# Kernel tuning notes

Measured on AMD Instinct MI355X. Metric: run time of the kernel, lower is better.

## Reference

```python
import jax, jax.numpy as jnp
import numpy as np

B, S, D = 4, 2048, 512   # batch, seq_len, hidden_size
H, HD = 1, 512           # num_heads (must be 1 given the view), head_size
ALPHA, BW, A = 2.0, 512.0, 0.5
EPS = 1e-12              # F.normalize / cdist-grad stabilizer


def setup_inputs() -> dict:
    key = jax.random.key(0)
    ks = jax.random.split(key, 7)
    s = 1.0 / np.sqrt(D)  # keep q,k,v at unit scale like trained weights
    return {
        "x": jax.random.normal(ks[0], (B, S, D), jnp.float32),
        "Wq": jax.random.normal(ks[1], (HD, D), jnp.float32) * s,
        "bq": jax.random.normal(ks[2], (HD,), jnp.float32) * 0.01,
        "Wk": jax.random.normal(ks[3], (HD, D), jnp.float32) * s,
        "bk": jax.random.normal(ks[4], (HD,), jnp.float32) * 0.01,
        "Wv": jax.random.normal(ks[5], (HD, D), jnp.float32) * s,
        "bv": jax.random.normal(ks[6], (HD,), jnp.float32) * 0.01,
    }


def reference(x, Wq, bq, Wk, bk, Wv, bv):
    # projections, then (B, H, S, HD)
    q = (x @ Wq.T + bq).reshape(B, S, H, HD).transpose(0, 2, 1, 3)
    k = (x @ Wk.T + bk).reshape(B, S, H, HD).transpose(0, 2, 1, 3)
    v = (x @ Wv.T + bv).reshape(B, S, H, HD).transpose(0, 2, 1, 3)

    # torch.cdist(q, k, p=2): pairwise Euclidean distance, shape (B, H, S, S)
    sq = ((q * q).sum(-1)[..., :, None]
          + (k * k).sum(-1)[..., None, :]
          - 2.0 * jnp.einsum('bhsd,bhtd->bhst', q, k))
    g_dist = jnp.sqrt(jnp.maximum(sq, EPS))

    # alpha >= 2 branch: exp(-(g / sqrt(bw))**(alpha/(alpha-1)))
    attn_score = jnp.exp(-(g_dist / jnp.sqrt(BW)) ** (ALPHA / (ALPHA - 1.0)))

    # bistochastic (Sinkhorn-like) renormalization, a > 0 branch
    N_R = attn_score.sum(-1)   # row sums  (B, H, S)
    N_C = attn_score.sum(-2)   # col sums  (B, H, S)
    K_tilde = (N_R ** (-A))[..., :, None] * attn_score * (N_C ** (-A))[..., None, :]

    # F.normalize(K_tilde, p=1, dim=3); entries are nonnegative so |.| == .
    probs = K_tilde / jnp.maximum(K_tilde.sum(-1, keepdims=True), EPS)

    # dropout prob = 0.0 -> identity
    out = jnp.einsum('bhst,bhtd->bhsd', probs, v)
    return out, probs
```

## Files before the change

### kernel.cpp

```cpp
#include <hip/hip_runtime.h>
#include <hip/hip_bf16.h>

typedef short short8 __attribute__((ext_vector_type(8)));
typedef short short4v __attribute__((ext_vector_type(4)));
typedef float f32x4 __attribute__((ext_vector_type(4)));

#define S_LEN 2048
#define DIM   512
#define NBATCH 4

typedef unsigned short ushort_t;

__device__ __forceinline__ float b2f(unsigned short u) {
    union { unsigned u; float f; } x; x.u = ((unsigned)u) << 16; return x.f;
}
__device__ __forceinline__ unsigned short f2b(float f) {
    union { float f; unsigned u; } x; x.f = f;
    unsigned r = x.u + 0x7FFFu + ((x.u >> 16) & 1u);
    return (unsigned short)(r >> 16);
}
__device__ __forceinline__ float wave_sum(float v) {
    #pragma unroll
    for (int off = 32; off > 0; off >>= 1) v += __shfl_xor(v, off, 64);
    return v;
}
__device__ __forceinline__ void gld16(const void* g, void* l) {
    __builtin_amdgcn_global_load_lds(
        (const __attribute__((address_space(1))) unsigned int*)g,
        (__attribute__((address_space(3))) unsigned int*)l, 16, 0, 0);
}

__global__ void convert_kernel(const float* __restrict__ x,
                               const float* __restrict__ Wq,
                               const float* __restrict__ Wk,
                               const float* __restrict__ Wv,
                               ushort_t* __restrict__ xb,
                               ushort_t* __restrict__ Wb)
{
    const int blk = blockIdx.x;
    const float* src;
    ushort_t* dst;
    size_t off;
    if (blk < 2048) {
        src = x; dst = xb; off = (size_t)blk * 2048;
    } else {
        int w = (blk - 2048) >> 7;
        int r = (blk - 2048) & 127;
        src = (w == 0) ? Wq : (w == 1) ? Wk : Wv;
        dst = Wb + (size_t)w * DIM * DIM;
        off = (size_t)r * 2048;
    }
    size_t i = off + (size_t)threadIdx.x * 8;
    f32x4 a = *(const f32x4*)&src[i];
    f32x4 c = *(const f32x4*)&src[i + 4];
    short8 o;
    #pragma unroll
    for (int e = 0; e < 4; e++) {
        o[e]     = (short)f2b(a[e]);
        o[4 + e] = (short)f2b(c[e]);
    }
    *(short8*)&dst[i] = o;
}

__global__ void proj_kernel(
    const ushort_t* __restrict__ xb,
    const ushort_t* __restrict__ Wb,
    const float* __restrict__ bq, const float* __restrict__ bk,
    const float* __restrict__ bv,
    ushort_t* __restrict__ Q, ushort_t* __restrict__ Kp,
    ushort_t* __restrict__ Vt)
{
    __shared__ __align__(16) ushort_t As[128 * 32];
    __shared__ __align__(16) ushort_t Bs[128 * 32];
    const int z = blockIdx.z;
    const ushort_t* A  = xb;
    const ushort_t* Bt = Wb + (size_t)z * DIM * DIM;
    const float* bias = (z == 0) ? bq : (z == 1) ? bk : bv;

    const int bm0 = blockIdx.x * 128, bn0 = blockIdx.y * 128;
    const int tid = threadIdx.x;
    const int lane = tid & 63, wave = tid >> 6;
    const int wm = wave >> 1, wn = wave & 1;
    const int quad = lane >> 4;
    const int mrow = wm * 64 + (lane & 15);
    const int ncol = wn * 64 + (lane & 15);
    f32x4 acc[4][4] = {};

    for (int k0 = 0; k0 < DIM; k0 += 32) {
        __syncthreads();
        #pragma unroll
        for (int u = 0; u < 2; u++) {
            int f = u * 256 + tid;
            int row = f >> 2, c4 = (f & 3) ^ ((row >> 1) & 3);
            gld16(&A[(size_t)(bm0 + row) * DIM + k0 + c4 * 8],
                  &As[(u * 256 + wave * 64) * 8]);
        }
        #pragma unroll
        for (int u = 0; u < 2; u++) {
            int f = u * 256 + tid;
            int row = f >> 2, c4 = (f & 3) ^ ((row >> 1) & 3);
            gld16(&Bt[(size_t)(bn0 + row) * DIM + k0 + c4 * 8],
                  &Bs[(u * 256 + wave * 64) * 8]);
        }
        __syncthreads();

        short8 af[4], bf[4];
        #pragma unroll
        for (int i = 0; i < 4; i++) {
            int row = mrow + 16 * i;
            af[i] = *(const short8*)&As[row * 32 + (quad ^ ((row >> 1) & 3)) * 8];
        }
        #pragma unroll
        for (int j = 0; j < 4; j++) {
            int row = ncol + 16 * j;
            bf[j] = *(const short8*)&Bs[row * 32 + (quad ^ ((row >> 1) & 3)) * 8];
        }
        #pragma unroll
        for (int i = 0; i < 4; i++)
            #pragma unroll
            for (int j = 0; j < 4; j++)
                acc[i][j] = __builtin_amdgcn_mfma_f32_16x16x32_bf16(
                    af[i], bf[j], acc[i][j], 0, 0, 0);
    }

    if (z < 2) {
        ushort_t* O = (z == 0) ? Q : Kp;
        #pragma unroll
        for (int j = 0; j < 4; j++) {
            int gcol = bn0 + wn * 64 + 16 * j + (lane & 15);
            float bb = bias[gcol];
            #pragma unroll
            for (int i = 0; i < 4; i++)
                #pragma unroll
                for (int r = 0; r < 4; r++) {
                    int grow = bm0 + wm * 64 + 16 * i + quad * 4 + r;
                    O[(size_t)grow * DIM + gcol] = f2b(acc[i][j][r] + bb);
                }
        }
    } else {
        #pragma unroll
        for (int j = 0; j < 4; j++) {
            int gcol = bn0 + wn * 64 + 16 * j + (lane & 15);
            float bb = bias[gcol];
            #pragma unroll
            for (int i = 0; i < 4; i++) {
                int grow0 = bm0 + wm * 64 + 16 * i + quad * 4;
                int bb2 = grow0 >> 11, s = grow0 & 2047;
                short4v o4;
                #pragma unroll
                for (int r = 0; r < 4; r++) o4[r] = (short)f2b(acc[i][j][r] + bb);
                *(short4v*)&Vt[((size_t)bb2 * DIM + gcol) * S_LEN + s] = o4;
            }
        }
    }
}

__global__ void norms_kernel(const ushort_t* __restrict__ Q,
                             const ushort_t* __restrict__ Kp,
                             float* __restrict__ nq, float* __restrict__ nk)
{
    const int wave = threadIdx.x >> 6, lane = threadIdx.x & 63;
    const int row = blockIdx.x * 4 + wave;
    const ushort_t* src = (blockIdx.y == 0) ? Q : Kp;
    float* dst = (blockIdx.y == 0) ? nq : nk;
    short8 v = *(const short8*)&src[(size_t)row * DIM + lane * 8];
    float s = 0.f;
    #pragma unroll
    for (int e = 0; e < 8; e++) { float f = b2f((ushort_t)v[e]); s += f * f; }
    s = wave_sum(s);
    if (lane == 0) dst[row] = s;
}

__global__ void score_kernel(const ushort_t* __restrict__ Q,
                             const ushort_t* __restrict__ Kp,
                             const float* __restrict__ nq,
                             const float* __restrict__ nk,
                             ushort_t* __restrict__ attnb,
                             float* __restrict__ NC)
{
    __shared__ __align__(16) ushort_t As[128 * 32];
    __shared__ __align__(16) ushort_t Bs[128 * 32];
    const int b = blockIdx.z;
    const ushort_t* A  = Q  + (size_t)b * S_LEN * DIM;
    const ushort_t* Bt = Kp + (size_t)b * S_LEN * DIM;
    const int bm0 = blockIdx.x * 128, bn0 = blockIdx.y * 128;
    const int tid = threadIdx.x;
    const int lane = tid & 63, wave = tid >> 6;
    const int wm = wave >> 1, wn = wave & 1;
    const int quad = lane >> 4;
    const int mrow = wm * 64 + (lane & 15);
    const int ncol = wn * 64 + (lane & 15);
    f32x4 acc[4][4] = {};

    for (int k0 = 0; k0 < DIM; k0 += 32) {
        __syncthreads();
        #pragma unroll
        for (int u = 0; u < 2; u++) {
            int f = u * 256 + tid;
            int row = f >> 2, c4 = (f & 3) ^ ((row >> 1) & 3);
            gld16(&A[(size_t)(bm0 + row) * DIM + k0 + c4 * 8],
                  &As[(u * 256 + wave * 64) * 8]);
        }
        #pragma unroll
        for (int u = 0; u < 2; u++) {
            int f = u * 256 + tid;
            int row = f >> 2, c4 = (f & 3) ^ ((row >> 1) & 3);
            gld16(&Bt[(size_t)(bn0 + row) * DIM + k0 + c4 * 8],
                  &Bs[(u * 256 + wave * 64) * 8]);
        }
        __syncthreads();

        short8 af[4], bf[4];
        #pragma unroll
        for (int i = 0; i < 4; i++) {
            int row = mrow + 16 * i;
            af[i] = *(const short8*)&As[row * 32 + (quad ^ ((row >> 1) & 3)) * 8];
        }
        #pragma unroll
        for (int j = 0; j < 4; j++) {
            int row = ncol + 16 * j;
            bf[j] = *(const short8*)&Bs[row * 32 + (quad ^ ((row >> 1) & 3)) * 8];
        }
        #pragma unroll
        for (int i = 0; i < 4; i++)
            #pragma unroll
            for (int j = 0; j < 4; j++)
                acc[i][j] = __builtin_amdgcn_mfma_f32_16x16x32_bf16(
                    af[i], bf[j], acc[i][j], 0, 0, 0);
    }

    ushort_t* ob = attnb + (size_t)b * S_LEN * S_LEN;
    float nqv[16], nkv[4];
    #pragma unroll
    for (int i = 0; i < 4; i++)
        #pragma unroll
        for (int r = 0; r < 4; r++)
            nqv[i * 4 + r] = nq[b * S_LEN + bm0 + wm * 64 + 16 * i + quad * 4 + r];
    #pragma unroll
    for (int j = 0; j < 4; j++)
        nkv[j] = nk[b * S_LEN + bn0 + wn * 64 + 16 * j + (lane & 15)];

    float cp[4] = {0.f, 0.f, 0.f, 0.f};
    #pragma unroll
    for (int i = 0; i < 4; i++)
        #pragma unroll
        for (int j = 0; j < 4; j++)
            #pragma unroll
            for (int r = 0; r < 4; r++) {
                int grow = bm0 + wm * 64 + 16 * i + quad * 4 + r;
                int gcol = bn0 + wn * 64 + 16 * j + (lane & 15);
                float sq = nqv[i * 4 + r] + nkv[j] - 2.0f * acc[i][j][r];
                sq = fmaxf(sq, 1e-12f);
                ushort_t ub = f2b(__expf(sq * (-1.0f / 512.0f)));
                ob[(size_t)grow * S_LEN + gcol] = ub;
                cp[j] += b2f(ub);
            }
    #pragma unroll
    for (int j = 0; j < 4; j++) {
        float v = cp[j];
        v += __shfl_xor(v, 16, 64);
        v += __shfl_xor(v, 32, 64);
        if (quad == 0) {
            int gcol = bn0 + wn * 64 + 16 * j + (lane & 15);
            atomicAdd(&NC[b * S_LEN + gcol], v);
        }
    }
}

__global__ void scale_vt_kernel(ushort_t* __restrict__ Vt,
                                const float* __restrict__ NC)
{
    size_t idx = ((size_t)blockIdx.x * 256 + threadIdx.x) * 8;
    int s0 = (int)(idx & 2047);
    int b  = (int)(idx >> 20);
    const float* cb = NC + (b << 11);
    short8 v = *(short8*)&Vt[idx];
    #pragma unroll
    for (int e = 0; e < 8; e++)
        v[e] = (short)f2b(b2f((ushort_t)v[e]) * rsqrtf(cb[s0 + e]));
    *(short8*)&Vt[idx] = v;
}

__global__ void rowsumprobs_kernel(const ushort_t* __restrict__ attnb,
                                   const float* __restrict__ NC,
                                   float* __restrict__ probs,
                                   float* __restrict__ rr)
{
    __shared__ float red[4];
    const int s = blockIdx.x, b = blockIdx.y;
    const size_t R = (size_t)b * S_LEN + s;
    const ushort_t* row = attnb + R * S_LEN;
    const float* cb = NC + (b << 11);
    const int t = threadIdx.x * 8;
    const int wave = threadIdx.x >> 6, lane = threadIdx.x & 63;

    short8 av = *(const short8*)&row[t];
    float pv[8], acc = 0.f;
    #pragma unroll
    for (int e = 0; e < 8; e++) {
        pv[e] = b2f((ushort_t)av[e]) * rsqrtf(cb[t + e]);
        acc += pv[e];
    }
    acc = wave_sum(acc);
    if (lane == 0) red[wave] = acc;
    __syncthreads();
    float rs = 1.0f / (red[0] + red[1] + red[2] + red[3]);

    float* prow = probs + R * S_LEN;
    f32x4 o0, o1;
    #pragma unroll
    for (int e = 0; e < 4; e++) { o0[e] = pv[e] * rs; o1[e] = pv[4 + e] * rs; }
    *(f32x4*)&prow[t] = o0;
    *(f32x4*)&prow[t + 4] = o1;
    if (threadIdx.x == 0) rr[R] = rs;
}

__global__ void out_gemm_kernel(const ushort_t* __restrict__ attnb,
                                const ushort_t* __restrict__ Vtc,
                                const float* __restrict__ rr,
                                float* __restrict__ outp)
{
    __shared__ __align__(16) ushort_t As[128 * 32];
    __shared__ __align__(16) ushort_t Bs[128 * 32];
    const int b = blockIdx.z;
    const ushort_t* A  = attnb + (size_t)b * S_LEN * S_LEN;
    const ushort_t* Bt = Vtc + (size_t)b * DIM * S_LEN;
    const int bm0 = blockIdx.x * 128, bn0 = blockIdx.y * 128;
    const int tid = threadIdx.x;
    const int lane = tid & 63, wave = tid >> 6;
    const int wm = wave >> 1, wn = wave & 1;
    const int quad = lane >> 4;
    const int mrow = wm * 64 + (lane & 15);
    const int ncol = wn * 64 + (lane & 15);
    f32x4 acc[4][4] = {};

    for (int k0 = 0; k0 < S_LEN; k0 += 32) {
        __syncthreads();
        #pragma unroll
        for (int u = 0; u < 2; u++) {
            int f = u * 256 + tid;
            int row = f >> 2, c4 = (f & 3) ^ ((row >> 1) & 3);
            gld16(&A[(size_t)(bm0 + row) * S_LEN + k0 + c4 * 8],
                  &As[(u * 256 + wave * 64) * 8]);
        }
        #pragma unroll
        for (int u = 0; u < 2; u++) {
            int f = u * 256 + tid;
            int row = f >> 2, c4 = (f & 3) ^ ((row >> 1) & 3);
            gld16(&Bt[(size_t)(bn0 + row) * S_LEN + k0 + c4 * 8],
                  &Bs[(u * 256 + wave * 64) * 8]);
        }
        __syncthreads();

        short8 af[4], bf[4];
        #pragma unroll
        for (int i = 0; i < 4; i++) {
            int row = mrow + 16 * i;
            af[i] = *(const short8*)&As[row * 32 + (quad ^ ((row >> 1) & 3)) * 8];
        }
        #pragma unroll
        for (int j = 0; j < 4; j++) {
            int row = ncol + 16 * j;
            bf[j] = *(const short8*)&Bs[row * 32 + (quad ^ ((row >> 1) & 3)) * 8];
        }
        #pragma unroll
        for (int i = 0; i < 4; i++)
            #pragma unroll
            for (int j = 0; j < 4; j++)
                acc[i][j] = __builtin_amdgcn_mfma_f32_16x16x32_bf16(
                    af[i], bf[j], acc[i][j], 0, 0, 0);
    }

    float* C = outp + (size_t)b * S_LEN * DIM;
    float rv[16];
    #pragma unroll
    for (int i = 0; i < 4; i++)
        #pragma unroll
        for (int r = 0; r < 4; r++)
            rv[i * 4 + r] = rr[b * S_LEN + bm0 + wm * 64 + 16 * i + quad * 4 + r];
    #pragma unroll
    for (int j = 0; j < 4; j++) {
        int gcol = bn0 + wn * 64 + 16 * j + (lane & 15);
        #pragma unroll
        for (int i = 0; i < 4; i++)
            #pragma unroll
            for (int r = 0; r < 4; r++) {
                int grow = bm0 + wm * 64 + 16 * i + quad * 4 + r;
                C[(size_t)grow * DIM + gcol] = acc[i][j][r] * rv[i * 4 + r];
            }
    }
}

extern "C" void kernel_launch(void* const* d_in, const int* in_sizes, int n_in,
                              void* d_out, int out_size, void* d_ws, size_t ws_size,
                              hipStream_t stream)
{
    const float* x  = (const float*)d_in[0];
    const float* Wq = (const float*)d_in[1];
    const float* bq = (const float*)d_in[2];
    const float* Wk = (const float*)d_in[3];
    const float* bk = (const float*)d_in[4];
    const float* Wv = (const float*)d_in[5];
    const float* bv = (const float*)d_in[6];

    float* out   = (float*)d_out;
    float* probs = out + (size_t)NBATCH * S_LEN * DIM;

    ushort_t* Qb = (ushort_t*)d_out;
    ushort_t* Kb = Qb + (size_t)8192 * DIM;
    ushort_t* xb = (ushort_t*)probs;
    ushort_t* Wb = xb + (size_t)8192 * DIM;
    ushort_t* Vt    = (ushort_t*)d_ws;
    ushort_t* attnb = Vt + (size_t)NBATCH * DIM * S_LEN;
    float* nq = (float*)(attnb + (size_t)NBATCH * S_LEN * S_LEN);
    float* nk = nq + 8192;
    float* NC = nk + 8192;
    float* cc = NC + 8192;
    float* rr = cc + 8192;

    hipMemsetAsync(NC, 0, 8192 * sizeof(float), stream);

    convert_kernel<<<2432, 256, 0, stream>>>(x, Wq, Wk, Wv, xb, Wb);
    proj_kernel<<<dim3(64, 4, 3), 256, 0, stream>>>(xb, Wb, bq, bk, bv,
                                                    Qb, Kb, Vt);
    norms_kernel<<<dim3(2048, 2), 256, 0, stream>>>(Qb, Kb, nq, nk);
    score_kernel<<<dim3(16, 16, NBATCH), 256, 0, stream>>>(Qb, Kb, nq, nk,
                                                           attnb, NC);
    scale_vt_kernel<<<2048, 256, 0, stream>>>(Vt, NC);
    rowsumprobs_kernel<<<dim3(S_LEN, NBATCH), 256, 0, stream>>>(attnb, NC,
                                                                probs, rr);
    out_gemm_kernel<<<dim3(16, 4, NBATCH), 256, 0, stream>>>(attnb, Vt, rr, out);
}
```

Before: 211.3 us.

## Double-buffer GEMM smem loads, widen out GEMM to 8 waves, nontemporal stores

```diff
diff --git a/kernel.cpp b/kernel.cpp
--- a/kernel.cpp
+++ b/kernel.cpp
@@ -70,8 +70,8 @@
     ushort_t* __restrict__ Q, ushort_t* __restrict__ Kp,
     ushort_t* __restrict__ Vt)
 {
-    __shared__ __align__(16) ushort_t As[128 * 32];
-    __shared__ __align__(16) ushort_t Bs[128 * 32];
+    __shared__ __align__(16) ushort_t As[2][128 * 32];
+    __shared__ __align__(16) ushort_t Bs[2][128 * 32];
     const int z = blockIdx.z;
     const ushort_t* A  = xb;
     const ushort_t* Bt = Wb + (size_t)z * DIM * DIM;
@@ -86,34 +86,38 @@
     const int ncol = wn * 64 + (lane & 15);
     f32x4 acc[4][4] = {};
 
-    for (int k0 = 0; k0 < DIM; k0 += 32) {
-        __syncthreads();
+    auto stage = [&](int cur, int k0) {
         #pragma unroll
         for (int u = 0; u < 2; u++) {
             int f = u * 256 + tid;
             int row = f >> 2, c4 = (f & 3) ^ ((row >> 1) & 3);
             gld16(&A[(size_t)(bm0 + row) * DIM + k0 + c4 * 8],
-                  &As[(u * 256 + wave * 64) * 8]);
+                  &As[cur][(u * 256 + wave * 64) * 8]);
         }
         #pragma unroll
         for (int u = 0; u < 2; u++) {
             int f = u * 256 + tid;
             int row = f >> 2, c4 = (f & 3) ^ ((row >> 1) & 3);
             gld16(&Bt[(size_t)(bn0 + row) * DIM + k0 + c4 * 8],
-                  &Bs[(u * 256 + wave * 64) * 8]);
-        }
-        __syncthreads();
-
+                  &Bs[cur][(u * 256 + wave * 64) * 8]);
+        }
+    };
+
+    stage(0, 0);
+    __syncthreads();
+    int cur = 0;
+    for (int t = 0; t < 16; t++) {
+        if (t + 1 < 16) stage(cur ^ 1, (t + 1) * 32);
         short8 af[4], bf[4];
         #pragma unroll
         for (int i = 0; i < 4; i++) {
             int row = mrow + 16 * i;
-            af[i] = *(const short8*)&As[row * 32 + (quad ^ ((row >> 1) & 3)) * 8];
+            af[i] = *(const short8*)&As[cur][row * 32 + (quad ^ ((row >> 1) & 3)) * 8];
         }
         #pragma unroll
         for (int j = 0; j < 4; j++) {
             int row = ncol + 16 * j;
-            bf[j] = *(const short8*)&Bs[row * 32 + (quad ^ ((row >> 1) & 3)) * 8];
+            bf[j] = *(const short8*)&Bs[cur][row * 32 + (quad ^ ((row >> 1) & 3)) * 8];
         }
         #pragma unroll
         for (int i = 0; i < 4; i++)
@@ -121,6 +125,8 @@
             for (int j = 0; j < 4; j++)
                 acc[i][j] = __builtin_amdgcn_mfma_f32_16x16x32_bf16(
                     af[i], bf[j], acc[i][j], 0, 0, 0);
+        __syncthreads();
+        cur ^= 1;
     }
 
     if (z < 2) {
@@ -178,8 +184,8 @@
                              ushort_t* __restrict__ attnb,
                              float* __restrict__ NC)
 {
-    __shared__ __align__(16) ushort_t As[128 * 32];
-    __shared__ __align__(16) ushort_t Bs[128 * 32];
+    __shared__ __align__(16) ushort_t As[2][128 * 32];
+    __shared__ __align__(16) ushort_t Bs[2][128 * 32];
     const int b = blockIdx.z;
     const ushort_t* A  = Q  + (size_t)b * S_LEN * DIM;
     const ushort_t* Bt = Kp + (size_t)b * S_LEN * DIM;
@@ -192,34 +198,38 @@
     const int ncol = wn * 64 + (lane & 15);
     f32x4 acc[4][4] = {};
 
-    for (int k0 = 0; k0 < DIM; k0 += 32) {
-        __syncthreads();
+    auto stage = [&](int cur, int k0) {
         #pragma unroll
         for (int u = 0; u < 2; u++) {
             int f = u * 256 + tid;
             int row = f >> 2, c4 = (f & 3) ^ ((row >> 1) & 3);
             gld16(&A[(size_t)(bm0 + row) * DIM + k0 + c4 * 8],
-                  &As[(u * 256 + wave * 64) * 8]);
+                  &As[cur][(u * 256 + wave * 64) * 8]);
         }
         #pragma unroll
         for (int u = 0; u < 2; u++) {
             int f = u * 256 + tid;
             int row = f >> 2, c4 = (f & 3) ^ ((row >> 1) & 3);
             gld16(&Bt[(size_t)(bn0 + row) * DIM + k0 + c4 * 8],
-                  &Bs[(u * 256 + wave * 64) * 8]);
-        }
-        __syncthreads();
-
+                  &Bs[cur][(u * 256 + wave * 64) * 8]);
+        }
+    };
+
+    stage(0, 0);
+    __syncthreads();
+    int cur = 0;
+    for (int t = 0; t < 16; t++) {
+        if (t + 1 < 16) stage(cur ^ 1, (t + 1) * 32);
         short8 af[4], bf[4];
         #pragma unroll
         for (int i = 0; i < 4; i++) {
             int row = mrow + 16 * i;
-            af[i] = *(const short8*)&As[row * 32 + (quad ^ ((row >> 1) & 3)) * 8];
+            af[i] = *(const short8*)&As[cur][row * 32 + (quad ^ ((row >> 1) & 3)) * 8];
         }
         #pragma unroll
         for (int j = 0; j < 4; j++) {
             int row = ncol + 16 * j;
-            bf[j] = *(const short8*)&Bs[row * 32 + (quad ^ ((row >> 1) & 3)) * 8];
+            bf[j] = *(const short8*)&Bs[cur][row * 32 + (quad ^ ((row >> 1) & 3)) * 8];
         }
         #pragma unroll
         for (int i = 0; i < 4; i++)
@@ -227,6 +237,8 @@
             for (int j = 0; j < 4; j++)
                 acc[i][j] = __builtin_amdgcn_mfma_f32_16x16x32_bf16(
                     af[i], bf[j], acc[i][j], 0, 0, 0);
+        __syncthreads();
+        cur ^= 1;
     }
 
     ushort_t* ob = attnb + (size_t)b * S_LEN * S_LEN;
@@ -310,8 +322,8 @@
     f32x4 o0, o1;
     #pragma unroll
     for (int e = 0; e < 4; e++) { o0[e] = pv[e] * rs; o1[e] = pv[4 + e] * rs; }
-    *(f32x4*)&prow[t] = o0;
-    *(f32x4*)&prow[t + 4] = o1;
+    __builtin_nontemporal_store(o0, (f32x4*)&prow[t]);
+    __builtin_nontemporal_store(o1, (f32x4*)&prow[t + 4]);
     if (threadIdx.x == 0) rr[R] = rs;
 }
 
@@ -320,74 +332,77 @@
                                 const float* __restrict__ rr,
                                 float* __restrict__ outp)
 {
-    __shared__ __align__(16) ushort_t As[128 * 32];
-    __shared__ __align__(16) ushort_t Bs[128 * 32];
+    __shared__ __align__(16) ushort_t As[2][128 * 32];
+    __shared__ __align__(16) ushort_t Bs[2][128 * 32];
     const int b = blockIdx.z;
     const ushort_t* A  = attnb + (size_t)b * S_LEN * S_LEN;
     const ushort_t* Bt = Vtc + (size_t)b * DIM * S_LEN;
     const int bm0 = blockIdx.x * 128, bn0 = blockIdx.y * 128;
     const int tid = threadIdx.x;
     const int lane = tid & 63, wave = tid >> 6;
-    const int wm = wave >> 1, wn = wave & 1;
+    const int wm = wave >> 2, wn = wave & 3;
     const int quad = lane >> 4;
     const int mrow = wm * 64 + (lane & 15);
-    const int ncol = wn * 64 + (lane & 15);
-    f32x4 acc[4][4] = {};
-
-    for (int k0 = 0; k0 < S_LEN; k0 += 32) {
-        __syncthreads();
-        #pragma unroll
-        for (int u = 0; u < 2; u++) {
-            int f = u * 256 + tid;
+    const int ncol = wn * 32 + (lane & 15);
+    f32x4 acc[4][2] = {};
+
+    auto stage = [&](int cur, int k0) {
+        {
+            int f = tid;
             int row = f >> 2, c4 = (f & 3) ^ ((row >> 1) & 3);
             gld16(&A[(size_t)(bm0 + row) * S_LEN + k0 + c4 * 8],
-                  &As[(u * 256 + wave * 64) * 8]);
-        }
-        #pragma unroll
-        for (int u = 0; u < 2; u++) {
-            int f = u * 256 + tid;
+                  &As[cur][(wave * 64) * 8]);
+        }
+        {
+            int f = tid;
             int row = f >> 2, c4 = (f & 3) ^ ((row >> 1) & 3);
             gld16(&Bt[(size_t)(bn0 + row) * S_LEN + k0 + c4 * 8],
-                  &Bs[(u * 256 + wave * 64) * 8]);
-        }
-        __syncthreads();
-
-        short8 af[4], bf[4];
+                  &Bs[cur][(wave * 64) * 8]);
+        }
+    };
+
+    stage(0, 0);
+    __syncthreads();
+    int cur = 0;
+    for (int t = 0; t < 64; t++) {
+        if (t + 1 < 64) stage(cur ^ 1, (t + 1) * 32);
+        short8 af[4], bf[2];
         #pragma unroll
         for (int i = 0; i < 4; i++) {
             int row = mrow + 16 * i;
-            af[i] = *(const short8*)&As[row * 32 + (quad ^ ((row >> 1) & 3)) * 8];
-        }
-        #pragma unroll
-        for (int j = 0; j < 4; j++) {
+            af[i] = *(const short8*)&As[cur][row * 32 + (quad ^ ((row >> 1) & 3)) * 8];
+        }
+        #pragma unroll
+        for (int j = 0; j < 2; j++) {
             int row = ncol + 16 * j;
-            bf[j] = *(const short8*)&Bs[row * 32 + (quad ^ ((row >> 1) & 3)) * 8];
+            bf[j] = *(const short8*)&Bs[cur][row * 32 + (quad ^ ((row >> 1) & 3)) * 8];
         }
         #pragma unroll
         for (int i = 0; i < 4; i++)
             #pragma unroll
-            for (int j = 0; j < 4; j++)
+            for (int j = 0; j < 2; j++)
                 acc[i][j] = __builtin_amdgcn_mfma_f32_16x16x32_bf16(
-                    af[i], bf[j], acc[i][j], 0, 0, 0);
+                    bf[j], af[i], acc[i][j], 0, 0, 0);
+        __syncthreads();
+        cur ^= 1;
     }
 
     float* C = outp + (size_t)b * S_LEN * DIM;
-    float rv[16];
+    float rv[4];
     #pragma unroll
     for (int i = 0; i < 4; i++)
-        #pragma unroll
-        for (int r = 0; r < 4; r++)
-            rv[i * 4 + r] = rr[b * S_LEN + bm0 + wm * 64 + 16 * i + quad * 4 + r];
-    #pragma unroll
-    for (int j = 0; j < 4; j++) {
-        int gcol = bn0 + wn * 64 + 16 * j + (lane & 15);
-        #pragma unroll
-        for (int i = 0; i < 4; i++)
-            #pragma unroll
-            for (int r = 0; r < 4; r++) {
-                int grow = bm0 + wm * 64 + 16 * i + quad * 4 + r;
-                C[(size_t)grow * DIM + gcol] = acc[i][j][r] * rv[i * 4 + r];
-            }
+        rv[i] = rr[b * S_LEN + bm0 + wm * 64 + 16 * i + (lane & 15)];
+    #pragma unroll
+    for (int i = 0; i < 4; i++) {
+        int grow = bm0 + wm * 64 + 16 * i + (lane & 15);
+        #pragma unroll
+        for (int j = 0; j < 2; j++) {
+            int gc = bn0 + wn * 32 + 16 * j + quad * 4;
+            f32x4 o;
+            #pragma unroll
+            for (int r = 0; r < 4; r++) o[r] = acc[i][j][r] * rv[i];
+            __builtin_nontemporal_store(o, (f32x4*)&C[(size_t)grow * DIM + gc]);
+        }
     }
 }
 
@@ -429,5 +444,5 @@
     scale_vt_kernel<<<2048, 256, 0, stream>>>(Vt, NC);
     rowsumprobs_kernel<<<dim3(S_LEN, NBATCH), 256, 0, stream>>>(attnb, NC,
                                                                 probs, rr);
-    out_gemm_kernel<<<dim3(16, 4, NBATCH), 256, 0, stream>>>(attnb, Vt, rr, out);
-}
+    out_gemm_kernel<<<dim3(16, 4, NBATCH), 512, 0, stream>>>(attnb, Vt, rr, out);
+}
```

Result: no change. 214.9 us (+1.7%).

## Fuse norms into projection, merge scale/rowsum kernels, retile output GEMM

Applied to the files above, without the earlier changes.

```diff
diff --git a/kernel.cpp b/kernel.cpp
--- a/kernel.cpp
+++ b/kernel.cpp
@@ -68,7 +68,8 @@
     const float* __restrict__ bq, const float* __restrict__ bk,
     const float* __restrict__ bv,
     ushort_t* __restrict__ Q, ushort_t* __restrict__ Kp,
-    ushort_t* __restrict__ Vt)
+    ushort_t* __restrict__ Vt,
+    float* __restrict__ nq, float* __restrict__ nk)
 {
     __shared__ __align__(16) ushort_t As[128 * 32];
     __shared__ __align__(16) ushort_t Bs[128 * 32];
@@ -125,6 +126,8 @@
 
     if (z < 2) {
         ushort_t* O = (z == 0) ? Q : Kp;
+        float* nrm  = (z == 0) ? nq : nk;
+        float ss[16] = {};
         #pragma unroll
         for (int j = 0; j < 4; j++) {
             int gcol = bn0 + wn * 64 + 16 * j + (lane & 15);
@@ -134,9 +137,26 @@
                 #pragma unroll
                 for (int r = 0; r < 4; r++) {
                     int grow = bm0 + wm * 64 + 16 * i + quad * 4 + r;
-                    O[(size_t)grow * DIM + gcol] = f2b(acc[i][j][r] + bb);
+                    ushort_t ub = f2b(acc[i][j][r] + bb);
+                    O[(size_t)grow * DIM + gcol] = ub;
+                    float vr = b2f(ub);
+                    ss[i * 4 + r] += vr * vr;
                 }
         }
+        #pragma unroll
+        for (int i = 0; i < 4; i++)
+            #pragma unroll
+            for (int r = 0; r < 4; r++) {
+                float s = ss[i * 4 + r];
+                s += __shfl_xor(s, 1, 64);
+                s += __shfl_xor(s, 2, 64);
+                s += __shfl_xor(s, 4, 64);
+                s += __shfl_xor(s, 8, 64);
+                if ((lane & 15) == 0) {
+                    int grow = bm0 + wm * 64 + 16 * i + quad * 4 + r;
+                    atomicAdd(&nrm[grow], s);
+                }
+            }
     } else {
         #pragma unroll
         for (int j = 0; j < 4; j++) {
@@ -153,22 +173,6 @@
             }
         }
     }
-}
-
-__global__ void norms_kernel(const ushort_t* __restrict__ Q,
-                             const ushort_t* __restrict__ Kp,
-                             float* __restrict__ nq, float* __restrict__ nk)
-{
-    const int wave = threadIdx.x >> 6, lane = threadIdx.x & 63;
-    const int row = blockIdx.x * 4 + wave;
-    const ushort_t* src = (blockIdx.y == 0) ? Q : Kp;
-    float* dst = (blockIdx.y == 0) ? nq : nk;
-    short8 v = *(const short8*)&src[(size_t)row * DIM + lane * 8];
-    float s = 0.f;
-    #pragma unroll
-    for (int e = 0; e < 8; e++) { float f = b2f((ushort_t)v[e]); s += f * f; }
-    s = wave_sum(s);
-    if (lane == 0) dst[row] = s;
 }
 
 __global__ void score_kernel(const ushort_t* __restrict__ Q,
@@ -267,52 +271,55 @@
     }
 }
 
-__global__ void scale_vt_kernel(ushort_t* __restrict__ Vt,
-                                const float* __restrict__ NC)
-{
-    size_t idx = ((size_t)blockIdx.x * 256 + threadIdx.x) * 8;
-    int s0 = (int)(idx & 2047);
-    int b  = (int)(idx >> 20);
-    const float* cb = NC + (b << 11);
-    short8 v = *(short8*)&Vt[idx];
-    #pragma unroll
-    for (int e = 0; e < 8; e++)
-        v[e] = (short)f2b(b2f((ushort_t)v[e]) * rsqrtf(cb[s0 + e]));
-    *(short8*)&Vt[idx] = v;
-}
-
-__global__ void rowsumprobs_kernel(const ushort_t* __restrict__ attnb,
-                                   const float* __restrict__ NC,
-                                   float* __restrict__ probs,
-                                   float* __restrict__ rr)
-{
-    __shared__ float red[4];
-    const int s = blockIdx.x, b = blockIdx.y;
+__global__ void scale_rowsum_kernel(ushort_t* __restrict__ Vt,
+                                    const float* __restrict__ NC,
+                                    const ushort_t* __restrict__ attnb,
+                                    float* __restrict__ probs,
+                                    float* __restrict__ rr)
+{
+    if (blockIdx.x >= 256) {
+        int vb = (blockIdx.x - 256) * 4 + blockIdx.y;
+        size_t idx = ((size_t)vb * 512 + threadIdx.x) * 8;
+        int s0 = (int)(idx & 2047);
+        int b  = (int)(idx >> 20);
+        const float* cb = NC + (b << 11);
+        short8 v = *(short8*)&Vt[idx];
+        #pragma unroll
+        for (int e = 0; e < 8; e++)
+            v[e] = (short)f2b(b2f((ushort_t)v[e]) * rsqrtf(cb[s0 + e]));
+        *(short8*)&Vt[idx] = v;
+        return;
+    }
+    const int wave = threadIdx.x >> 6, lane = threadIdx.x & 63;
+    const int s = blockIdx.x * 8 + wave, b = blockIdx.y;
     const size_t R = (size_t)b * S_LEN + s;
     const ushort_t* row = attnb + R * S_LEN;
     const float* cb = NC + (b << 11);
-    const int t = threadIdx.x * 8;
-    const int wave = threadIdx.x >> 6, lane = threadIdx.x & 63;
-
-    short8 av = *(const short8*)&row[t];
-    float pv[8], acc = 0.f;
-    #pragma unroll
-    for (int e = 0; e < 8; e++) {
-        pv[e] = b2f((ushort_t)av[e]) * rsqrtf(cb[t + e]);
-        acc += pv[e];
-    }
-    acc = wave_sum(acc);
-    if (lane == 0) red[wave] = acc;
-    __syncthreads();
-    float rs = 1.0f / (red[0] + red[1] + red[2] + red[3]);
+
+    float pv[4][8], acc = 0.f;
+    #pragma unroll
+    for (int c = 0; c < 4; c++) {
+        int t = c * 512 + lane * 8;
+        short8 av = *(const short8*)&row[t];
+        #pragma unroll
+        for (int e = 0; e < 8; e++) {
+            pv[c][e] = b2f((ushort_t)av[e]) * rsqrtf(cb[t + e]);
+            acc += pv[c][e];
+        }
+    }
+    float rs = 1.0f / wave_sum(acc);
 
     float* prow = probs + R * S_LEN;
-    f32x4 o0, o1;
-    #pragma unroll
-    for (int e = 0; e < 4; e++) { o0[e] = pv[e] * rs; o1[e] = pv[4 + e] * rs; }
-    *(f32x4*)&prow[t] = o0;
-    *(f32x4*)&prow[t + 4] = o1;
-    if (threadIdx.x == 0) rr[R] = rs;
+    #pragma unroll
+    for (int c = 0; c < 4; c++) {
+        int t = c * 512 + lane * 8;
+        f32x4 o0, o1;
+        #pragma unroll
+        for (int e = 0; e < 4; e++) { o0[e] = pv[c][e] * rs; o1[e] = pv[c][4 + e] * rs; }
+        __builtin_nontemporal_store(o0, (f32x4*)&prow[t]);
+        __builtin_nontemporal_store(o1, (f32x4*)&prow[t + 4]);
+    }
+    if (lane == 0) rr[R] = rs;
 }
 
 __global__ void out_gemm_kernel(const ushort_t* __restrict__ attnb,
@@ -328,66 +335,64 @@
     const int bm0 = blockIdx.x * 128, bn0 = blockIdx.y * 128;
     const int tid = threadIdx.x;
     const int lane = tid & 63, wave = tid >> 6;
-    const int wm = wave >> 1, wn = wave & 1;
+    const int wm = wave >> 2, wn = wave & 3;
     const int quad = lane >> 4;
     const int mrow = wm * 64 + (lane & 15);
-    const int ncol = wn * 64 + (lane & 15);
-    f32x4 acc[4][4] = {};
+    const int ncol = wn * 32 + (lane & 15);
+    f32x4 acc[4][2] = {};
 
     for (int k0 = 0; k0 < S_LEN; k0 += 32) {
         __syncthreads();
-        #pragma unroll
-        for (int u = 0; u < 2; u++) {
-            int f = u * 256 + tid;
+        {
+            int f = tid;
             int row = f >> 2, c4 = (f & 3) ^ ((row >> 1) & 3);
             gld16(&A[(size_t)(bm0 + row) * S_LEN + k0 + c4 * 8],
-                  &As[(u * 256 + wave * 64) * 8]);
-        }
-        #pragma unroll
-        for (int u = 0; u < 2; u++) {
-            int f = u * 256 + tid;
+                  &As[(wave * 64) * 8]);
+        }
+        {
+            int f = tid;
             int row = f >> 2, c4 = (f & 3) ^ ((row >> 1) & 3);
             gld16(&Bt[(size_t)(bn0 + row) * S_LEN + k0 + c4 * 8],
-                  &Bs[(u * 256 + wave * 64) * 8]);
-        }
-        __syncthreads();
-
-        short8 af[4], bf[4];
+                  &Bs[(wave * 64) * 8]);
+        }
+        __syncthreads();
+
+        short8 af[4], bf[2];
         #pragma unroll
         for (int i = 0; i < 4; i++) {
             int row = mrow + 16 * i;
             af[i] = *(const short8*)&As[row * 32 + (quad ^ ((row >> 1) & 3)) * 8];
         }
         #pragma unroll
-        for (int j = 0; j < 4; j++) {
+        for (int j = 0; j < 2; j++) {
             int row = ncol + 16 * j;
             bf[j] = *(const short8*)&Bs[row * 32 + (quad ^ ((row >> 1) & 3)) * 8];
         }
         #pragma unroll
         for (int i = 0; i < 4; i++)
             #pragma unroll
-            for (int j = 0; j < 4; j++)
+            for (int j = 0; j < 2; j++)
                 acc[i][j] = __builtin_amdgcn_mfma_f32_16x16x32_bf16(
-                    af[i], bf[j], acc[i][j], 0, 0, 0);
+                    bf[j], af[i], acc[i][j], 0, 0, 0);
+        __syncthreads();
     }
 
     float* C = outp + (size_t)b * S_LEN * DIM;
-    float rv[16];
+    float rv[4];
     #pragma unroll
     for (int i = 0; i < 4; i++)
-        #pragma unroll
-        for (int r = 0; r < 4; r++)
-            rv[i * 4 + r] = rr[b * S_LEN + bm0 + wm * 64 + 16 * i + quad * 4 + r];
-    #pragma unroll
-    for (int j = 0; j < 4; j++) {
-        int gcol = bn0 + wn * 64 + 16 * j + (lane & 15);
-        #pragma unroll
-        for (int i = 0; i < 4; i++)
-            #pragma unroll
-            for (int r = 0; r < 4; r++) {
-                int grow = bm0 + wm * 64 + 16 * i + quad * 4 + r;
-                C[(size_t)grow * DIM + gcol] = acc[i][j][r] * rv[i * 4 + r];
-            }
+        rv[i] = rr[b * S_LEN + bm0 + wm * 64 + 16 * i + (lane & 15)];
+    #pragma unroll
+    for (int i = 0; i < 4; i++) {
+        int grow = bm0 + wm * 64 + 16 * i + (lane & 15);
+        #pragma unroll
+        for (int j = 0; j < 2; j++) {
+            int gc = bn0 + wn * 32 + 16 * j + quad * 4;
+            f32x4 o;
+            #pragma unroll
+            for (int r = 0; r < 4; r++) o[r] = acc[i][j][r] * rv[i];
+            __builtin_nontemporal_store(o, (f32x4*)&C[(size_t)grow * DIM + gc]);
+        }
     }
 }
 
@@ -418,16 +423,14 @@
     float* cc = NC + 8192;
     float* rr = cc + 8192;
 
-    hipMemsetAsync(NC, 0, 8192 * sizeof(float), stream);
+    hipMemsetAsync(nq, 0, 3 * 8192 * sizeof(float), stream);
 
     convert_kernel<<<2432, 256, 0, stream>>>(x, Wq, Wk, Wv, xb, Wb);
     proj_kernel<<<dim3(64, 4, 3), 256, 0, stream>>>(xb, Wb, bq, bk, bv,
-                                                    Qb, Kb, Vt);
-    norms_kernel<<<dim3(2048, 2), 256, 0, stream>>>(Qb, Kb, nq, nk);
+                                                    Qb, Kb, Vt, nq, nk);
     score_kernel<<<dim3(16, 16, NBATCH), 256, 0, stream>>>(Qb, Kb, nq, nk,
                                                            attnb, NC);
-    scale_vt_kernel<<<2048, 256, 0, stream>>>(Vt, NC);
-    rowsumprobs_kernel<<<dim3(S_LEN, NBATCH), 256, 0, stream>>>(attnb, NC,
-                                                                probs, rr);
-    out_gemm_kernel<<<dim3(16, 4, NBATCH), 256, 0, stream>>>(attnb, Vt, rr, out);
-}
+    scale_rowsum_kernel<<<dim3(512, NBATCH), 512, 0, stream>>>(Vt, NC, attnb,
+                                                               probs, rr);
+    out_gemm_kernel<<<dim3(16, 4, NBATCH), 512, 0, stream>>>(attnb, Vt, rr, out);
+}
```

After: 209.5 us. Within noise of the previous version (-0.9%).
